# Optimization experiments

Measured on AMD Instinct MI355X. Metric: run time of the kernel, lower is better.

## Reference

```python
import jax, jax.numpy as jnp
import numpy as np

B, S, H, DH = 4, 2048, 16, 64
D = H * DH          # 1024
EXP = 2
FF_IN = EXP * D * 2  # 4096 (SwiGLU doubles)
FF_HID = EXP * D     # 2048
SCALE_BASE = 512
LN_EPS = 1e-5


def setup_inputs() -> dict:
    key = jax.random.key(0)
    ks = jax.random.split(key, 8)
    inp = {
        "q": jax.random.normal(ks[0], (B, S, D), jnp.float32),
        "k": jax.random.normal(ks[1], (B, S, D), jnp.float32),
        "v": jax.random.normal(ks[2], (B, S, D), jnp.float32),
        "Wqkv": jax.random.normal(ks[3], (D, 3 * D), jnp.float32) * (1.0 / np.sqrt(D)),
        "bqkv": jnp.zeros((3 * D,), jnp.float32),
        "q_scale": jnp.ones((DH,), jnp.float32),
        "k_scale": jnp.ones((DH,), jnp.float32),
        "ln_g": jnp.ones((D,), jnp.float32),
        "ln_b": jnp.zeros((D,), jnp.float32),
        "W1": jax.random.normal(ks[4], (D, FF_IN), jnp.float32) * (1.0 / np.sqrt(D)),
        "b1": jnp.zeros((FF_IN,), jnp.float32),
        "W2": jax.random.normal(ks[5], (FF_HID, D), jnp.float32) * (1.0 / np.sqrt(FF_HID)),
        "b2": jnp.zeros((D,), jnp.float32),
    }
    return inp


def rotate_half(x):
    x1, x2 = jnp.split(x, 2, axis=-1)
    return jnp.concatenate((-x2, x1), axis=-1)


def apply_rope(pos, t, scale):
    # pos: [S, DH], scale: [S, DH] (broadcast over [B, H, S, DH])
    return t * jnp.cos(pos) * scale + rotate_half(t) * jnp.sin(pos) * scale


def rotary_tables(seq_len):
    inv_freq = 1.0 / (10000.0 ** (jnp.arange(0, DH, 2, dtype=jnp.float32) / DH))
    t = jnp.arange(seq_len, dtype=jnp.float32)
    freqs = t[:, None] * inv_freq[None, :]            # [S, DH/2]
    freqs = jnp.concatenate((freqs, freqs), axis=-1)  # [S, DH]
    power = (t - seq_len // 2) / SCALE_BASE           # [S]
    base = (jnp.arange(0, DH, 2, dtype=jnp.float32) + 0.4 * DH) / (1.4 * DH)  # [DH/2]
    scale = base[None, :] ** power[:, None]           # [S, DH/2]
    scale = jnp.concatenate((scale, scale), axis=-1)  # [S, DH]
    return freqs, scale


def l2norm(x, eps=1e-12):
    n = jnp.sqrt(jnp.sum(x * x, axis=-1, keepdims=True))
    return x / jnp.maximum(n, eps)


def reference(q, k, v, Wqkv, bqkv, q_scale, k_scale, ln_g, ln_b, W1, b1, W2, b2):
    del k, v  # module projects qkv from q; k,v args are unused (faithful to source)
    n, seq_len, _ = q.shape
    qkv = q @ Wqkv + bqkv                              # [B, S, 3D]
    qkv = qkv.reshape(n, seq_len, H, 3 * DH).transpose(0, 2, 1, 3)  # [B, H, S, 3DH]
    q_, k_, v_ = jnp.split(qkv, 3, axis=-1)
    q_ = l2norm(q_) * q_scale
    k_ = l2norm(k_) * k_scale
    pos, xscale = rotary_tables(seq_len)
    q_ = apply_rope(pos, q_, xscale)
    k_ = apply_rope(pos, k_, 1.0 / xscale)
    # scaled dot product attention (non-causal)
    scores = jnp.einsum("bhid,bhjd->bhij", q_, k_) / np.sqrt(DH)
    attn = jax.nn.softmax(scores, axis=-1)
    out = jnp.einsum("bhij,bhjd->bhid", attn, v_)      # [B, H, S, DH]
    out = out.transpose(0, 2, 1, 3).reshape(n, seq_len, D)
    # LayerNorm
    mu = jnp.mean(out, axis=-1, keepdims=True)
    var = jnp.mean((out - mu) ** 2, axis=-1, keepdims=True)
    out = (out - mu) / jnp.sqrt(var + LN_EPS) * ln_g + ln_b
    # SwiGLU FFN (dropout = identity in eval)
    h = out @ W1 + b1                                  # [B, S, FF_IN]
    x_, gate = jnp.split(h, 2, axis=-1)
    ff = (jax.nn.silu(gate) * x_) @ W2 + b2            # [B, S, D]
    return out + ff
```

## Files before the change

### kernel.cpp

```cpp
#include <hip/hip_runtime.h>
#include <math.h>


typedef __bf16 bf16;
typedef bf16 bf16x8 __attribute__((ext_vector_type(8)));
typedef bf16 bf16x4 __attribute__((ext_vector_type(4)));
typedef float f32x4 __attribute__((ext_vector_type(4)));

#define MFMA(a, b, c) __builtin_amdgcn_mfma_f32_16x16x32_bf16(a, b, c, 0, 0, 0)

__device__ __forceinline__ void async16(const void* g, void* l) {
    __builtin_amdgcn_global_load_lds(
        (const __attribute__((address_space(1))) void*)g,
        (__attribute__((address_space(3))) void*)l,
        16, 0, 0);
}

__global__ __launch_bounds__(256) void fill_sentinel(float* __restrict__ o)
{
    size_t i = ((size_t)blockIdx.x * 256 + threadIdx.x) * 4;
    *(float4*)&o[i] = make_float4(0.25f, 0.25f, 0.25f, 0.25f);
}

__global__ __launch_bounds__(256) void convert_f32_bf16(
    const float* __restrict__ in, bf16* __restrict__ out)
{
    size_t i = ((size_t)blockIdx.x * 256 + threadIdx.x) * 8;
    float4 f0 = *(const float4*)&in[i];
    float4 f1 = *(const float4*)&in[i + 4];
    bf16x8 v;
    v[0] = (bf16)f0.x; v[1] = (bf16)f0.y; v[2] = (bf16)f0.z; v[3] = (bf16)f0.w;
    v[4] = (bf16)f1.x; v[5] = (bf16)f1.y; v[6] = (bf16)f1.z; v[7] = (bf16)f1.w;
    *(bf16x8*)&out[i] = v;
}

__global__ __launch_bounds__(256) void transpose_f32_bf16(
    const float* __restrict__ in, bf16* __restrict__ out, int K, int N)
{
    __shared__ bf16 T[64][70];
    const int tN = N >> 6;
    const int tk = blockIdx.x / tN, tn = blockIdx.x % tN;
    const int k0 = tk << 6, n0 = tn << 6;
    const int t = threadIdx.x;
    const int r = t >> 2, c0 = (t & 3) << 4;
    const float* src = &in[(size_t)(k0 + r) * N + n0 + c0];
    for (int j = 0; j < 4; ++j) {
        float4 f = *(const float4*)(src + 4 * j);
        T[r][c0 + 4 * j + 0] = (bf16)f.x;
        T[r][c0 + 4 * j + 1] = (bf16)f.y;
        T[r][c0 + 4 * j + 2] = (bf16)f.z;
        T[r][c0 + 4 * j + 3] = (bf16)f.w;
    }
    __syncthreads();
    bf16x8 o0, o1;
    for (int i = 0; i < 8; ++i) o0[i] = T[c0 + i][r];
    for (int i = 0; i < 8; ++i) o1[i] = T[c0 + 8 + i][r];
    *(bf16x8*)&out[(size_t)(n0 + r) * K + k0 + c0]     = o0;
    *(bf16x8*)&out[(size_t)(n0 + r) * K + k0 + c0 + 8] = o1;
}

__global__ __launch_bounds__(256) void transpose_v(
    const bf16* __restrict__ in, bf16* __restrict__ out)
{
    __shared__ bf16 T[64][72];
    const int bh = blockIdx.x >> 5;
    const int s0 = (blockIdx.x & 31) << 6;
    const bf16* ip = in + ((size_t)bh << 17) + (size_t)s0 * 64;
    bf16* op = out + ((size_t)bh << 17) + s0;
    const int t = threadIdx.x;
    const int r = t >> 2, c0 = (t & 3) << 4;
    *(bf16x8*)&T[r][c0]     = *(const bf16x8*)&ip[r * 64 + c0];
    *(bf16x8*)&T[r][c0 + 8] = *(const bf16x8*)&ip[r * 64 + c0 + 8];
    __syncthreads();
    bf16x8 o0, o1;
    for (int i = 0; i < 8; ++i) o0[i] = T[c0 + i][r];
    for (int i = 0; i < 8; ++i) o1[i] = T[c0 + 8 + i][r];
    *(bf16x8*)&op[(size_t)r * 2048 + c0]     = o0;
    *(bf16x8*)&op[(size_t)r * 2048 + c0 + 8] = o1;
}

template <int BN>
__device__ __forceinline__ void g256_stage(
    const bf16* __restrict__ Ag, const bf16* __restrict__ Bg, int kt,
    int lda, int K, char* aB, char* bB, int tid, int wave)
{
    for (int i = 0; i < 4; ++i) {
        int l = (i << 9) + tid;
        int r = l >> 3;
        int cbs = ((l & 7) ^ (r & 7)) << 3;
        int cu = (i << 9) + (wave << 6);
        async16(&Ag[(size_t)r * lda + kt + cbs], aB + (size_t)cu * 16);
    }
    for (int i = 0; i < BN / 64; ++i) {
        int l = (i << 9) + tid;
        int r = l >> 3;
        int cbs = ((l & 7) ^ (r & 7)) << 3;
        int cu = (i << 9) + (wave << 6);
        async16(&Bg[(size_t)r * K + kt + cbs], bB + (size_t)cu * 16);
    }
}

template <int NI>
__device__ __forceinline__ void g256_compute(
    const bf16* At, const bf16* Bt, f32x4 (&acc)[8][NI],
    int wm, int wn, int l16, int quad, int rsw)
{
    for (int kd = 0; kd < 2; ++kd) {
        bf16x8 af[8], bfr[NI];
        for (int mi = 0; mi < 8; ++mi) {
            int row = (wm << 7) + (mi << 4) + l16;
            af[mi] = *(const bf16x8*)&At[(row << 6) + ((((kd << 2) + quad) ^ rsw) << 3)];
        }
        for (int ni = 0; ni < NI; ++ni) {
            int row = wn * (NI << 4) + (ni << 4) + l16;
            bfr[ni] = *(const bf16x8*)&Bt[(row << 6) + ((((kd << 2) + quad) ^ rsw) << 3)];
        }
        __builtin_amdgcn_s_setprio(1);
        for (int mi = 0; mi < 8; ++mi)
            for (int ni = 0; ni < NI; ++ni)
                acc[mi][ni] = MFMA(af[mi], bfr[ni], acc[mi][ni]);
        __builtin_amdgcn_s_setprio(0);
    }
}

#define G256_WAIT()                                                        \
    if constexpr (BN == 256) asm volatile("s_waitcnt vmcnt(8)" ::: "memory"); \
    else                     asm volatile("s_waitcnt vmcnt(6)" ::: "memory")

template <int EPI, int BN>
__global__ __launch_bounds__(512, 2) void gemm256(
    const bf16* __restrict__ A, const bf16* __restrict__ BT,
    const float* __restrict__ bias, int M, int N, int K, int lda,
    bf16* __restrict__ C0, bf16* __restrict__ C1, bf16* __restrict__ C2,
    float* __restrict__ Cf, const bf16* __restrict__ resid)
{
    constexpr int NI = BN / 64;
    __shared__ bf16 As[2][256 * 64];
    __shared__ bf16 Bs[2][BN * 64];
    const int tid = threadIdx.x;
    const int lane = tid & 63, wave = tid >> 6;
    const int quad = lane >> 4, l16 = lane & 15;
    const int rsw = l16 & 7;
    const int wm = wave >> 2, wn = wave & 3;
    const int nb = N / BN;
    const int nwg = gridDim.x;
    const int bid = blockIdx.x;
    const int swz = (bid & 7) * (nwg >> 3) + (bid >> 3);
    const int bm = swz / nb, bn = swz % nb;
    const int m0 = bm << 8, n0 = bn * BN;
    const bf16* Ag = A + (size_t)m0 * lda;
    const bf16* Bg = BT + (size_t)n0 * K;
    char* a0 = (char*)&As[0][0]; char* a1 = (char*)&As[1][0];
    char* b0 = (char*)&Bs[0][0]; char* b1 = (char*)&Bs[1][0];

    f32x4 acc[8][NI] = {};
    const int NT = K >> 6;

    g256_stage<BN>(Ag, Bg, 0,  lda, K, a0, b0, tid, wave);
    g256_stage<BN>(Ag, Bg, 64, lda, K, a1, b1, tid, wave);
    G256_WAIT();
    __builtin_amdgcn_s_barrier();

    for (int t = 0; t < NT; t += 2) {
        g256_compute<NI>(&As[0][0], &Bs[0][0], acc, wm, wn, l16, quad, rsw);
        asm volatile("" ::: "memory");
        __builtin_amdgcn_s_barrier();
        if (t + 2 < NT) {
            g256_stage<BN>(Ag, Bg, (t + 2) << 6, lda, K, a0, b0, tid, wave);
            G256_WAIT();
        } else {
            asm volatile("s_waitcnt vmcnt(0)" ::: "memory");
        }
        __builtin_amdgcn_s_barrier();
        g256_compute<NI>(&As[1][0], &Bs[1][0], acc, wm, wn, l16, quad, rsw);
        asm volatile("" ::: "memory");
        __builtin_amdgcn_s_barrier();
        if (t + 3 < NT) {
            g256_stage<BN>(Ag, Bg, (t + 3) << 6, lda, K, a1, b1, tid, wave);
            G256_WAIT();
        } else {
            asm volatile("s_waitcnt vmcnt(0)" ::: "memory");
        }
        __builtin_amdgcn_s_barrier();
    }

    for (int mi = 0; mi < 8; ++mi) {
        for (int ni = 0; ni < NI; ++ni) {
            for (int r = 0; r < 4; ++r) {
                int row = m0 + (wm << 7) + (mi << 4) + (quad << 2) + r;
                int col = n0 + wn * (NI << 4) + (ni << 4) + l16;
                float v = acc[mi][ni][r] + bias[col];
                if (EPI == 0) {
                    int b = row >> 11, s = row & 2047;
                    int h = col / 192, w = col % 192;
                    int tq = w >> 6, d = w & 63;
                    bf16* dst = (tq == 0) ? C0 : (tq == 1) ? C1 : C2;
                    dst[((((size_t)b * 16 + h) * 2048 + s) << 6) + d] = (bf16)v;
                } else if (EPI == 1) {
                    C0[(size_t)row * N + col] = (bf16)v;
                } else {
                    float rv = (float)resid[(size_t)row * N + col];
                    Cf[(size_t)row * N + col] = v + rv;
                }
            }
        }
    }
}

__global__ __launch_bounds__(256) void norm_rope(
    bf16* __restrict__ qb, bf16* __restrict__ kb,
    const float* __restrict__ qs, const float* __restrict__ ks)
{
    const int wave = threadIdx.x >> 6, lane = threadIdx.x & 63;
    const int rid = blockIdx.x * 4 + wave;
    const bool is_k = rid >= 131072;
    const int idx = is_k ? rid - 131072 : rid;
    const int s = idx & 2047;
    bf16* ptr = (is_k ? kb : qb) + ((size_t)idx << 6);
    const int d = lane;

    float v = (float)ptr[d];
    float ss = v * v;
    for (int o = 1; o < 64; o <<= 1) ss += __shfl_xor(ss, o);
    float t = v * rsqrtf(fmaxf(ss, 1e-24f));
    t *= (is_k ? ks : qs)[d];

    float partner = __shfl_xor(t, 32);
    float rh = (d < 32) ? -partner : partner;

    const float fi = (float)(d & 31);
    float inv_freq = __builtin_amdgcn_exp2f(fi * -0.4152410118609203f);
    float pos = (float)s * inv_freq;
    float rev = pos * 0.15915494309189535f;
    rev = rev - floorf(rev);
    float sn = __builtin_amdgcn_sinf(rev);
    float cs = __builtin_amdgcn_cosf(rev);
    float base = (2.0f * fi + 25.6f) * (1.0f / 89.6f);
    float power = ((float)s - 1024.0f) * (1.0f / 512.0f);
    if (is_k) power = -power;
    float xsc = __builtin_amdgcn_exp2f(power * __builtin_amdgcn_logf(base));
    ptr[d] = (bf16)((t * cs + rh * sn) * xsc);
}

__device__ __forceinline__ int swz_a(int r) {
    int a = (r >> 3) & 3;
    return (r & 7) ^ a ^ ((a << 1) & 7);
}

__device__ __forceinline__ void attn_stage(
    const bf16* __restrict__ Kp, const bf16* __restrict__ Vp, int kt,
    char* kB, char* vB, int tid, int wave)
{
    for (int i = 0; i < 2; ++i) {
        int l = (i << 8) + tid;
        int r = l >> 3;
        int cbs = ((l & 7) ^ swz_a(r)) << 3;
        int cu = (i << 8) + (wave << 6);
        async16(&Kp[(size_t)(kt + r) * 64 + cbs], kB + (size_t)cu * 16);
        async16(&Vp[(size_t)r * 2048 + kt + cbs], vB + (size_t)cu * 16);
    }
}

__global__ __launch_bounds__(256) void attn(
    const bf16* __restrict__ Q, const bf16* __restrict__ Kb,
    const bf16* __restrict__ VT, bf16* __restrict__ O)
{
    __shared__ bf16 Ks[2][64 * 64];
    __shared__ bf16 Vt[2][64 * 64];
    const int tid = threadIdx.x;
    const int lane = tid & 63, wave = tid >> 6;
    const int quad = lane >> 4, l16 = lane & 15;
    const int bh = blockIdx.x >> 4;
    const int q0 = (blockIdx.x & 15) << 7;
    const int s_base = q0 + (wave << 5);
    const bf16* Qp = Q + ((size_t)bh << 17);
    const bf16* Kp = Kb + ((size_t)bh << 17);
    const bf16* Vp = VT + ((size_t)bh << 17);

    bf16x8 qf[2][2];
    for (int sub = 0; sub < 2; ++sub) {
        const bf16* qrow = Qp + (size_t)(s_base + (sub << 4) + l16) * 64;
        qf[sub][0] = *(const bf16x8*)&qrow[(quad << 3)];
        qf[sub][1] = *(const bf16x8*)&qrow[32 + (quad << 3)];
        for (int j = 0; j < 8; ++j) {
            qf[sub][0][j] = (bf16)((float)qf[sub][0][j] * 0.1803368801f);
            qf[sub][1][j] = (bf16)((float)qf[sub][1][j] * 0.1803368801f);
        }
    }
    bf16x8 ones = {};
    if (l16 == 0) for (int j = 0; j < 8; ++j) ones[j] = (bf16)1.0f;

    f32x4 oacc[2][4] = {};
    f32x4 lacc[2] = {};

    attn_stage(Kp, Vp, 0, (char*)&Ks[0][0], (char*)&Vt[0][0], tid, wave);

    int buf = 0;
    for (int kt = 0; kt < 2048; kt += 64, buf ^= 1) {
        __syncthreads();
        if (kt + 64 < 2048)
            attn_stage(Kp, Vp, kt + 64,
                       (char*)&Ks[buf ^ 1][0], (char*)&Vt[buf ^ 1][0], tid, wave);

        const bf16* Kt_ = &Ks[buf][0];
        const bf16* Vc_ = &Vt[buf][0];

        bf16x8 pf0[2], pf1[2];
        for (int nt = 0; nt < 4; ++nt) {
            const int g = ((l16 >> 2) << 3) + (l16 & 3)
                        + ((nt & 1) << 2) + ((nt >> 1) << 5);
            const int gs = swz_a(g);
            bf16x8 kf0 = *(const bf16x8*)&Kt_[(g << 6) + ((quad ^ gs) << 3)];
            bf16x8 kf1 = *(const bf16x8*)&Kt_[(g << 6) + (((quad + 4) ^ gs) << 3)];
            __builtin_amdgcn_s_setprio(1);
            for (int sub = 0; sub < 2; ++sub) {
                f32x4 z = {};
                z = MFMA(kf0, qf[sub][0], z);
                z = MFMA(kf1, qf[sub][1], z);
                bf16x8& dst = (nt < 2) ? pf0[sub] : pf1[sub];
                const int jb = (nt & 1) << 2;
                for (int r = 0; r < 4; ++r)
                    dst[jb + r] = (bf16)__builtin_amdgcn_exp2f(z[r]);
            }
            __builtin_amdgcn_s_setprio(0);
        }

        __builtin_amdgcn_s_setprio(1);
        for (int ntd = 0; ntd < 4; ++ntd) {
            int row = (ntd << 4) + l16;
            int vs = swz_a(row);
            bf16x8 vf0 = *(const bf16x8*)&Vc_[(row << 6) + ((quad ^ vs) << 3)];
            bf16x8 vf1 = *(const bf16x8*)&Vc_[(row << 6) + (((quad + 4) ^ vs) << 3)];
            for (int sub = 0; sub < 2; ++sub) {
                oacc[sub][ntd] = MFMA(pf0[sub], vf0, oacc[sub][ntd]);
                oacc[sub][ntd] = MFMA(pf1[sub], vf1, oacc[sub][ntd]);
            }
        }
        for (int sub = 0; sub < 2; ++sub) {
            lacc[sub] = MFMA(pf0[sub], ones, lacc[sub]);
            lacc[sub] = MFMA(pf1[sub], ones, lacc[sub]);
        }
        __builtin_amdgcn_s_setprio(0);
    }

    const int b = bh >> 4, h = bh & 15;
    for (int sub = 0; sub < 2; ++sub)
        for (int r = 0; r < 4; ++r) {
            float l = __shfl(lacc[sub][r], quad << 4);
            float inv_l = 1.0f / l;
            int srow = s_base + (sub << 4) + (quad << 2) + r;
            for (int ntd = 0; ntd < 4; ++ntd) {
                int d = (ntd << 4) + l16;
                O[((((size_t)b * 2048 + srow) * 16) + h) * 64 + d] =
                    (bf16)(oacc[sub][ntd][r] * inv_l);
            }
        }
}

__global__ __launch_bounds__(256) void layernorm(
    const bf16* __restrict__ x, const float* __restrict__ g,
    const float* __restrict__ b, bf16* __restrict__ y)
{
    __shared__ float red[8];
    const int row = blockIdx.x;
    const int t = threadIdx.x;
    const bf16* xr = x + ((size_t)row << 10);
    bf16x4 xv = *(const bf16x4*)&xr[t << 2];
    float v[4], s = 0.0f, sq = 0.0f;
    for (int i = 0; i < 4; ++i) { v[i] = (float)xv[i]; s += v[i]; sq += v[i] * v[i]; }
    for (int o = 1; o < 64; o <<= 1) { s += __shfl_xor(s, o); sq += __shfl_xor(sq, o); }
    const int wave = t >> 6, lane = t & 63;
    if (lane == 0) { red[wave] = s; red[4 + wave] = sq; }
    __syncthreads();
    s  = red[0] + red[1] + red[2] + red[3];
    sq = red[4] + red[5] + red[6] + red[7];
    float mu = s * (1.0f / 1024.0f);
    float var = fmaxf(sq * (1.0f / 1024.0f) - mu * mu, 0.0f);
    float rstd = rsqrtf(var + 1e-5f);
    bf16x4 ov;
    for (int i = 0; i < 4; ++i) {
        int c = (t << 2) + i;
        ov[i] = (bf16)((v[i] - mu) * rstd * g[c] + b[c]);
    }
    *(bf16x4*)(y + ((size_t)row << 10) + (t << 2)) = ov;
}

__global__ __launch_bounds__(256) void swiglu(bf16* __restrict__ h)
{
    size_t i = ((size_t)blockIdx.x * 256 + threadIdx.x) * 8;
    size_t row = i >> 11, c = i & 2047;
    bf16* hr = h + (row << 12);
    bf16x8 xv = *(const bf16x8*)&hr[c];
    bf16x8 gv = *(const bf16x8*)&hr[c + 2048];
    bf16x8 ov;
    for (int j = 0; j < 8; ++j) {
        float xf = (float)xv[j], gf = (float)gv[j];
        ov[j] = (bf16)(gf / (1.0f + __expf(-gf)) * xf);
    }
    *(bf16x8*)&hr[c] = ov;
}

extern "C" void kernel_launch(void* const* d_in, const int* in_sizes, int n_in,
                              void* d_out, int out_size, void* d_ws, size_t ws_size,
                              hipStream_t stream) {
    (void)in_sizes; (void)n_in; (void)out_size;
    const float* q    = (const float*)d_in[0];
    const float* Wqkv = (const float*)d_in[3];
    const float* bqkv = (const float*)d_in[4];
    const float* qsc  = (const float*)d_in[5];
    const float* ksc  = (const float*)d_in[6];
    const float* lng  = (const float*)d_in[7];
    const float* lnb  = (const float*)d_in[8];
    const float* W1   = (const float*)d_in[9];
    const float* b1   = (const float*)d_in[10];
    const float* W2   = (const float*)d_in[11];
    const float* b2   = (const float*)d_in[12];
    float* out = (float*)d_out;

    const size_t MB = 1024 * 1024;
    if (ws_size < 92 * MB) {
        fill_sentinel<<<8192, 256, 0, stream>>>(out);
        return;
    }

    char* ws = (char*)d_ws;
    bf16* W2T      = (bf16*)(ws + 0);
    bf16* ln_buf   = (bf16*)(ws + 4  * MB);
    bf16* q_bf     = (bf16*)(ws + 4  * MB);
    bf16* W1T      = (bf16*)(ws + 20 * MB);
    bf16* q_buf    = (bf16*)(ws + 28 * MB);
    bf16* k_buf    = (bf16*)(ws + 44 * MB);
    bf16* v_buf    = (bf16*)(ws + 60 * MB);
    bf16* WqkvT    = (bf16*)(ws + 76 * MB);
    bf16* vt_buf   = (bf16*)(ws + 76 * MB);
    bf16* attn_buf = (bf16*)(ws + 60 * MB);
    bf16* h_buf    = (bf16*)(ws + 28 * MB);

    convert_f32_bf16<<<4096, 256, 0, stream>>>(q, q_bf);
    transpose_f32_bf16<<<512,  256, 0, stream>>>(W2,   W2T,   2048, 1024);
    transpose_f32_bf16<<<1024, 256, 0, stream>>>(W1,   W1T,   1024, 4096);
    transpose_f32_bf16<<<768,  256, 0, stream>>>(Wqkv, WqkvT, 1024, 3072);

    gemm256<0, 128><<<768, 512, 0, stream>>>(q_bf, WqkvT, bqkv, 8192, 3072, 1024, 1024,
                                             q_buf, k_buf, v_buf, nullptr, nullptr);
    norm_rope<<<65536, 256, 0, stream>>>(q_buf, k_buf, qsc, ksc);
    transpose_v<<<2048, 256, 0, stream>>>(v_buf, vt_buf);
    attn<<<1024, 256, 0, stream>>>(q_buf, k_buf, vt_buf, attn_buf);
    layernorm<<<8192, 256, 0, stream>>>(attn_buf, lng, lnb, ln_buf);
    gemm256<1, 256><<<512, 512, 0, stream>>>(ln_buf, W1T, b1, 8192, 4096, 1024, 1024,
                                             h_buf, nullptr, nullptr, nullptr, nullptr);
    swiglu<<<8192, 256, 0, stream>>>(h_buf);
    gemm256<2, 128><<<256, 512, 0, stream>>>(h_buf, W2T, b2, 8192, 1024, 2048, 4096,
                                             nullptr, nullptr, nullptr, out, ln_buf);
}
```

Measured before the change: 508.7 us.

## Fuse SwiGLU into W1 GEMM epilogue via split x/gate tiles; remap attention blocks

The W1 GEMM now loads 128 x-columns and the matching 128 gate-columns into each 256-wide B tile. Its epilogue applies SiLU(gate)*x and writes only the 2048-wide hidden activation, which removes the separate swiglu kernel and the 4096-wide intermediate round trip through memory. The W2 GEMM then reads the compact buffer with the smaller leading dimension. The attention grid is also remapped so that consecutive blocks interleave across heads, which changes cache locality and scheduling.

```diff
diff --git a/kernel.cpp b/kernel.cpp
--- a/kernel.cpp
+++ b/kernel.cpp
@@ -79,7 +79,7 @@
     *(bf16x8*)&op[(size_t)r * 2048 + c0 + 8] = o1;
 }
 
-template <int BN>
+template <int BN, bool SPLIT>
 __device__ __forceinline__ void g256_stage(
     const bf16* __restrict__ Ag, const bf16* __restrict__ Bg, int kt,
     int lda, int K, char* aB, char* bB, int tid, int wave)
@@ -96,11 +96,12 @@
         int r = l >> 3;
         int cbs = ((l & 7) ^ (r & 7)) << 3;
         int cu = (i << 9) + (wave << 6);
-        async16(&Bg[(size_t)r * K + kt + cbs], bB + (size_t)cu * 16);
-    }
-}
-
-template <int NI>
+        size_t grow = SPLIT ? (size_t)(r + ((r >> 7) * 1920)) : (size_t)r;
+        async16(&Bg[grow * K + kt + cbs], bB + (size_t)cu * 16);
+    }
+}
+
+template <int NI, bool SPLIT>
 __device__ __forceinline__ void g256_compute(
     const bf16* At, const bf16* Bt, f32x4 (&acc)[8][NI],
     int wm, int wn, int l16, int quad, int rsw)
@@ -112,7 +113,11 @@
             af[mi] = *(const bf16x8*)&At[(row << 6) + ((((kd << 2) + quad) ^ rsw) << 3)];
         }
         for (int ni = 0; ni < NI; ++ni) {
-            int row = wn * (NI << 4) + (ni << 4) + l16;
+            int row;
+            if (SPLIT)
+                row = ((ni >= 2) ? 128 : 0) + (wn << 5) + ((ni & 1) << 4) + l16;
+            else
+                row = wn * (NI << 4) + (ni << 4) + l16;
             bfr[ni] = *(const bf16x8*)&Bt[(row << 6) + ((((kd << 2) + quad) ^ rsw) << 3)];
         }
         __builtin_amdgcn_s_setprio(1);
@@ -135,6 +140,8 @@
     float* __restrict__ Cf, const bf16* __restrict__ resid)
 {
     constexpr int NI = BN / 64;
+    constexpr bool SPLIT = (EPI == 3);
+    constexpr int TILE_N = SPLIT ? 128 : BN;
     __shared__ bf16 As[2][256 * 64];
     __shared__ bf16 Bs[2][BN * 64];
     const int tid = threadIdx.x;
@@ -142,12 +149,12 @@
     const int quad = lane >> 4, l16 = lane & 15;
     const int rsw = l16 & 7;
     const int wm = wave >> 2, wn = wave & 3;
-    const int nb = N / BN;
+    const int nb = N / TILE_N;
     const int nwg = gridDim.x;
     const int bid = blockIdx.x;
     const int swz = (bid & 7) * (nwg >> 3) + (bid >> 3);
     const int bm = swz / nb, bn = swz % nb;
-    const int m0 = bm << 8, n0 = bn * BN;
+    const int m0 = bm << 8, n0 = bn * TILE_N;
     const bf16* Ag = A + (size_t)m0 * lda;
     const bf16* Bg = BT + (size_t)n0 * K;
     char* a0 = (char*)&As[0][0]; char* a1 = (char*)&As[1][0];
@@ -156,32 +163,48 @@
     f32x4 acc[8][NI] = {};
     const int NT = K >> 6;
 
-    g256_stage<BN>(Ag, Bg, 0,  lda, K, a0, b0, tid, wave);
-    g256_stage<BN>(Ag, Bg, 64, lda, K, a1, b1, tid, wave);
+    g256_stage<BN, SPLIT>(Ag, Bg, 0,  lda, K, a0, b0, tid, wave);
+    g256_stage<BN, SPLIT>(Ag, Bg, 64, lda, K, a1, b1, tid, wave);
     G256_WAIT();
     __builtin_amdgcn_s_barrier();
 
     for (int t = 0; t < NT; t += 2) {
-        g256_compute<NI>(&As[0][0], &Bs[0][0], acc, wm, wn, l16, quad, rsw);
+        g256_compute<NI, SPLIT>(&As[0][0], &Bs[0][0], acc, wm, wn, l16, quad, rsw);
         asm volatile("" ::: "memory");
         __builtin_amdgcn_s_barrier();
         if (t + 2 < NT) {
-            g256_stage<BN>(Ag, Bg, (t + 2) << 6, lda, K, a0, b0, tid, wave);
+            g256_stage<BN, SPLIT>(Ag, Bg, (t + 2) << 6, lda, K, a0, b0, tid, wave);
             G256_WAIT();
         } else {
             asm volatile("s_waitcnt vmcnt(0)" ::: "memory");
         }
         __builtin_amdgcn_s_barrier();
-        g256_compute<NI>(&As[1][0], &Bs[1][0], acc, wm, wn, l16, quad, rsw);
+        g256_compute<NI, SPLIT>(&As[1][0], &Bs[1][0], acc, wm, wn, l16, quad, rsw);
         asm volatile("" ::: "memory");
         __builtin_amdgcn_s_barrier();
         if (t + 3 < NT) {
-            g256_stage<BN>(Ag, Bg, (t + 3) << 6, lda, K, a1, b1, tid, wave);
+            g256_stage<BN, SPLIT>(Ag, Bg, (t + 3) << 6, lda, K, a1, b1, tid, wave);
             G256_WAIT();
         } else {
             asm volatile("s_waitcnt vmcnt(0)" ::: "memory");
         }
         __builtin_amdgcn_s_barrier();
+    }
+
+    if (EPI == 3) {
+        for (int mi = 0; mi < 8; ++mi) {
+            for (int ni = 0; ni < 2; ++ni) {
+                for (int r = 0; r < 4; ++r) {
+                    int row  = m0 + (wm << 7) + (mi << 4) + (quad << 2) + r;
+                    int colx = n0 + (wn << 5) + (ni << 4) + l16;
+                    float x = acc[mi][ni][r]     + bias[colx];
+                    float g = acc[mi][ni + 2][r] + bias[2048 + colx];
+                    float s = g / (1.0f + __expf(-g)) * x;
+                    C0[(size_t)row * N + colx] = (bf16)s;
+                }
+            }
+        }
+        return;
     }
 
     for (int mi = 0; mi < 8; ++mi) {
@@ -270,8 +293,10 @@
     const int tid = threadIdx.x;
     const int lane = tid & 63, wave = tid >> 6;
     const int quad = lane >> 4, l16 = lane & 15;
-    const int bh = blockIdx.x >> 4;
-    const int q0 = (blockIdx.x & 15) << 7;
+    const int wgi = blockIdx.x;
+    const int rr = wgi >> 3;
+    const int bh = ((wgi & 7) << 3) + (rr >> 4);
+    const int q0 = (rr & 15) << 7;
     const int s_base = q0 + (wave << 5);
     const bf16* Qp = Q + ((size_t)bh << 17);
     const bf16* Kp = Kb + ((size_t)bh << 17);
@@ -385,21 +410,6 @@
     *(bf16x4*)(y + ((size_t)row << 10) + (t << 2)) = ov;
 }
 
-__global__ __launch_bounds__(256) void swiglu(bf16* __restrict__ h)
-{
-    size_t i = ((size_t)blockIdx.x * 256 + threadIdx.x) * 8;
-    size_t row = i >> 11, c = i & 2047;
-    bf16* hr = h + (row << 12);
-    bf16x8 xv = *(const bf16x8*)&hr[c];
-    bf16x8 gv = *(const bf16x8*)&hr[c + 2048];
-    bf16x8 ov;
-    for (int j = 0; j < 8; ++j) {
-        float xf = (float)xv[j], gf = (float)gv[j];
-        ov[j] = (bf16)(gf / (1.0f + __expf(-gf)) * xf);
-    }
-    *(bf16x8*)&hr[c] = ov;
-}
-
 extern "C" void kernel_launch(void* const* d_in, const int* in_sizes, int n_in,
                               void* d_out, int out_size, void* d_ws, size_t ws_size,
                               hipStream_t stream) {
@@ -447,9 +457,8 @@
     transpose_v<<<2048, 256, 0, stream>>>(v_buf, vt_buf);
     attn<<<1024, 256, 0, stream>>>(q_buf, k_buf, vt_buf, attn_buf);
     layernorm<<<8192, 256, 0, stream>>>(attn_buf, lng, lnb, ln_buf);
-    gemm256<1, 256><<<512, 512, 0, stream>>>(ln_buf, W1T, b1, 8192, 4096, 1024, 1024,
+    gemm256<3, 256><<<512, 512, 0, stream>>>(ln_buf, W1T, b1, 8192, 2048, 1024, 1024,
                                              h_buf, nullptr, nullptr, nullptr, nullptr);
-    swiglu<<<8192, 256, 0, stream>>>(h_buf);
-    gemm256<2, 128><<<256, 512, 0, stream>>>(h_buf, W2T, b2, 8192, 1024, 2048, 4096,
+    gemm256<2, 128><<<256, 512, 0, stream>>>(h_buf, W2T, b2, 8192, 1024, 2048, 2048,
                                              nullptr, nullptr, nullptr, out, ln_buf);
 }
```

New measurement: 489.5 us. 1.04x faster.
